# Kernel optimization log

Hardware: AMD Instinct MI355X
Metric: run time of the kernel (lower is better)

## Reference

```python
import jax, jax.numpy as jnp
import numpy as np

D_MODEL = 1024
NUM_HEADS = 16


def setup_inputs() -> dict:
    key = jax.random.key(0)
    ks = jax.random.split(key, 5)
    sigma = (2.0 / (D_MODEL + D_MODEL)) ** 0.5
    def trunc(k):
        # truncated normal in [-3*sigma, 3*sigma], std sigma
        return sigma * jax.random.truncated_normal(k, -3.0, 3.0, (D_MODEL, D_MODEL), jnp.float32)
    x = jax.random.normal(ks[0], (4, 2048, D_MODEL), jnp.float32)
    return {
        "x": x,
        "W_Q": trunc(ks[1]),
        "W_K": trunc(ks[2]),
        "W_V": trunc(ks[3]),
        "W_O": trunc(ks[4]),
    }


def _mha(x, W_Q, W_K, W_V, W_O):
    B, S, D = x.shape
    H = NUM_HEADS
    dk = D // H
    # Linear stores W as (d_out, d_in); einsum '... d_in, d_out d_in -> ... d_out'
    Q = jnp.einsum('bsd,ed->bse', x, W_Q).reshape(B, S, H, dk).transpose(0, 2, 1, 3)
    K = jnp.einsum('bsd,ed->bse', x, W_K).reshape(B, S, H, dk).transpose(0, 2, 1, 3)
    V = jnp.einsum('bsd,ed->bse', x, W_V).reshape(B, S, H, dk).transpose(0, 2, 1, 3)
    scores = jnp.einsum('bhnd,bhmd->bhnm', Q, K) / jnp.sqrt(jnp.asarray(dk, x.dtype))
    causal = jnp.tril(jnp.ones((S, S), bool))
    scores = jnp.where(causal, scores, -jnp.inf)
    attn = jax.nn.softmax(scores, axis=-1)
    out = jnp.einsum('bhnm,bhmd->bhnd', attn, V)  # [B,H,S,dk]
    out = out.transpose(0, 2, 1, 3).reshape(B, S, D)
    return jnp.einsum('bsd,ed->bse', out, W_O)


def reference(x, W_Q, W_K, W_V, W_O):
    return _mha(x, W_Q, W_K, W_V, W_O)
```

## Files before the change

kernel.cpp:

```cpp
#include <hip/hip_runtime.h>
#include <hip/hip_bf16.h>
#include <stdint.h>


typedef unsigned short u16;
typedef short bf16x8 __attribute__((ext_vector_type(8)));
typedef float f32x4 __attribute__((ext_vector_type(4)));
typedef unsigned short u16x8 __attribute__((ext_vector_type(8)));

#define S_LEN 2048
#define DMODEL 1024
#define NH 16

__device__ __forceinline__ u16 f2bf(float f) {
    unsigned u = __builtin_bit_cast(unsigned, f);
    unsigned r = (u + 0x7fffu + ((u >> 16) & 1u)) >> 16;
    return (u16)r;
}

__device__ __forceinline__ float fast_exp2(float x) {
    return __builtin_amdgcn_exp2f(x);
}

__device__ __forceinline__ unsigned cvtpk_bf16(float lo, float hi_) {
    unsigned r;
    asm("v_cvt_pk_bf16_f32 %0, %1, %2" : "=v"(r) : "v"(lo), "v"(hi_));
    return r;
}

__device__ __forceinline__ void gll16(const void* g, void* s) {
    __builtin_amdgcn_global_load_lds((const __attribute__((address_space(1))) unsigned*)g,
                                     (__attribute__((address_space(3))) unsigned*)s, 16, 0, 0);
}

__global__ __launch_bounds__(256) void cast_all(
    const float* __restrict__ x, const float* __restrict__ wq, const float* __restrict__ wk,
    const float* __restrict__ wv, const float* __restrict__ wo,
    u16* __restrict__ xb, u16* __restrict__ wqkv, u16* __restrict__ wob, int nx) {
    const int NW = DMODEL * DMODEL;
    int i4 = (blockIdx.x * 256 + threadIdx.x) * 4;
    const float* src; u16* dst; int off;
    if (i4 < nx)             { src = x;  dst = xb;            off = i4; }
    else if (i4 < nx + NW)   { src = wq; dst = wqkv;          off = i4 - nx; }
    else if (i4 < nx + 2*NW) { src = wk; dst = wqkv + NW;     off = i4 - nx - NW; }
    else if (i4 < nx + 3*NW) { src = wv; dst = wqkv + 2*NW;   off = i4 - nx - 2*NW; }
    else                     { src = wo; dst = wob;           off = i4 - nx - 3*NW; }
    float4 v = *reinterpret_cast<const float4*>(src + off);
    ushort4 o4; o4.x = f2bf(v.x); o4.y = f2bf(v.y); o4.z = f2bf(v.z); o4.w = f2bf(v.w);
    *reinterpret_cast<ushort4*>(dst + off) = o4;
}

template <typename OUT>
__global__ __launch_bounds__(256) void gemm_bt(const u16* __restrict__ A, const u16* __restrict__ B,
                                               OUT* __restrict__ C, int M, int N, int K,
                                               int qcols, float qscale, u16* __restrict__ vt) {
    __shared__ u16 As[128 * 64];
    __shared__ u16 Bs[128 * 64];
    __shared__ u16 Ts[4][16 * 72];
    const int m0 = blockIdx.y * 128, n0 = blockIdx.x * 128;
    const int t = threadIdx.x, w = t >> 6, l = t & 63;
    const int hi = l >> 4;
    const int wr = w >> 1, wc = w & 1;
    f32x4 acc[4][4] = {};

    const int lr = l >> 3;
    const int lc = l & 7;
    const int gcol = (lc ^ lr) * 8;
    const u16* Ag = A + (size_t)(m0 + w * 32 + lr) * K + gcol;
    const u16* Bg = B + (size_t)(n0 + w * 32 + lr) * K + gcol;

    for (int k0 = 0; k0 < K; k0 += 64) {
        __syncthreads();
#pragma unroll
        for (int c = 0; c < 4; c++) {
            gll16(Ag + (size_t)c * 8 * K + k0, As + w * 2048 + c * 512);
            gll16(Bg + (size_t)c * 8 * K + k0, Bs + w * 2048 + c * 512);
        }
        __syncthreads();
#pragma unroll
        for (int kk = 0; kk < 2; kk++) {
            bf16x8 af[4], bfr[4];
#pragma unroll
            for (int mi = 0; mi < 4; mi++)
                af[mi] = *(const bf16x8*)&As[(wr * 64 + mi * 16 + (l & 15)) * 64 +
                                             (((kk * 4 + hi) ^ (l & 7)) * 8)];
#pragma unroll
            for (int ni = 0; ni < 4; ni++)
                bfr[ni] = *(const bf16x8*)&Bs[(wc * 64 + ni * 16 + (l & 15)) * 64 +
                                              (((kk * 4 + hi) ^ (l & 7)) * 8)];
#pragma unroll
            for (int mi = 0; mi < 4; mi++)
#pragma unroll
                for (int ni = 0; ni < 4; ni++)
                    acc[mi][ni] = __builtin_amdgcn_mfma_f32_16x16x32_bf16(af[mi], bfr[ni], acc[mi][ni], 0, 0, 0);
        }
    }

    if (vt != nullptr && n0 >= 2048) {
        const int mw = m0 + wr * 64;
        const int bq = mw >> 11;
        const int s0w = mw & (S_LEN - 1);
        const int hd = ((n0 + wc * 64) - 2048) >> 6;
        u16* tb = &Ts[w][0];
#pragma unroll
        for (int ni = 0; ni < 4; ni++) {
#pragma unroll
            for (int mi = 0; mi < 4; mi++) {
                uint2 pk = make_uint2(cvtpk_bf16(acc[mi][ni][0], acc[mi][ni][1]),
                                      cvtpk_bf16(acc[mi][ni][2], acc[mi][ni][3]));
                *(uint2*)&tb[(l & 15) * 72 + mi * 16 + hi * 4] = pk;
            }
            bf16x8 r0 = *(const bf16x8*)&tb[(l & 15) * 72 + hi * 16];
            bf16x8 r1 = *(const bf16x8*)&tb[(l & 15) * 72 + hi * 16 + 8];
            size_t vrow = ((size_t)(bq * 16 + hd) * 64 + ni * 16 + (l & 15)) * S_LEN + s0w + hi * 16;
            *(u16x8*)&vt[vrow]     = (u16x8)r0;
            *(u16x8*)&vt[vrow + 8] = (u16x8)r1;
        }
    } else {
#pragma unroll
        for (int mi = 0; mi < 4; mi++)
#pragma unroll
            for (int ni = 0; ni < 4; ni++)
#pragma unroll
                for (int j = 0; j < 4; j++) {
                    int r = m0 + wr * 64 + mi * 16 + hi * 4 + j;
                    int c = n0 + wc * 64 + ni * 16 + (l & 15);
                    float v = acc[mi][ni][j];
                    if (c < qcols) v *= qscale;
                    if constexpr (__is_same(OUT, u16)) C[(size_t)r * N + c] = f2bf(v);
                    else                               C[(size_t)r * N + c] = v;
                }
    }
}

__global__ __launch_bounds__(256, 2) void attn(const u16* __restrict__ QKV, const u16* __restrict__ VT,
                                               u16* __restrict__ O) {
    const int bh = blockIdx.x, y = blockIdx.y;
    const int qt = (y < 16) ? y : 47 - y;
    const int b = bh >> 4, h = bh & 15;
    const int t = threadIdx.x, w = t >> 6, l = t & 63;
    const int q = l & 15, hi = l >> 4, s7 = q & 7;

    __shared__ u16 SM[2][2][64][64];
    __shared__ u16 PS[4][16][64];

    const int srow = t >> 3, sblk = t & 7;
    const int gs = (sblk ^ (srow & 7)) * 8;
    const u16* Kg = QKV + (size_t)(b * S_LEN + srow) * 3072 + 1024 + h * 64 + gs;
    const u16* Vg = VT + (size_t)(bh * 64 + srow) * S_LEN + gs;
    const u16* Kg2 = Kg + (size_t)32 * 3072;
    const u16* Vg2 = Vg + (size_t)32 * S_LEN;

    const int kA0 = q * 128 + ((hi ^ s7) << 4);
    const int kA1 = kA0 ^ 64;
    const char* smbase = (const char*)&SM[0][0][0][0];

    char* pbase = (char*)&PS[w][0][0];
    const int pw0 = q * 128 + ((((0 * 2) + (hi >> 1)) ^ s7) << 4) + ((hi & 1) << 3);
    const int pw1 = q * 128 + ((((1 * 2) + (hi >> 1)) ^ s7) << 4) + ((hi & 1) << 3);
    const int pw2 = q * 128 + ((((2 * 2) + (hi >> 1)) ^ s7) << 4) + ((hi & 1) << 3);
    const int pw3 = q * 128 + ((((3 * 2) + (hi >> 1)) ^ s7) << 4) + ((hi & 1) << 3);
    const int pr0 = q * 128 + (((0 * 4 + hi) ^ s7) << 4);
    const int pr1 = q * 128 + (((1 * 4 + hi) ^ s7) << 4);

    const int q64 = qt * 64;
    const int nt = qt + 1;
    const int qglob = q64 + w * 16 + q;

    bf16x8 qf[2];
#pragma unroll
    for (int kk = 0; kk < 2; kk++)
        qf[kk] = *(const bf16x8*)&QKV[(size_t)(b * S_LEN + qglob) * 3072 + h * 64 + kk * 32 + hi * 8];

    f32x4 oacc[4] = {};
    float ss0 = 0.f, ss1 = 0.f;

    gll16(Kg,  (u16*)&SM[0][0][0][0] + t * 8);
    gll16(Kg2, (u16*)&SM[0][0][0][0] + 2048 + t * 8);
    gll16(Vg,  (u16*)&SM[0][1][0][0] + t * 8);
    gll16(Vg2, (u16*)&SM[0][1][0][0] + 2048 + t * 8);
    __syncthreads();

    const u16* KgT  = Kg  + (size_t)64 * 3072;
    const u16* Kg2T = Kg2 + (size_t)64 * 3072;
    const u16* VgT  = Vg  + 64;
    const u16* Vg2T = Vg2 + 64;

#pragma unroll 1
    for (int tt = 0; tt < nt; ++tt) {
        const int cur = tt & 1;
        if (tt + 1 < nt) {
            gll16(KgT,  (u16*)&SM[cur ^ 1][0][0][0] + t * 8);
            gll16(Kg2T, (u16*)&SM[cur ^ 1][0][0][0] + 2048 + t * 8);
            gll16(VgT,  (u16*)&SM[cur ^ 1][1][0][0] + t * 8);
            gll16(Vg2T, (u16*)&SM[cur ^ 1][1][0][0] + 2048 + t * 8);
            KgT  += (size_t)64 * 3072;
            Kg2T += (size_t)64 * 3072;
            VgT  += 64;
            Vg2T += 64;
        }
        const int kv0 = tt * 64;
        const char* kb = smbase + cur * 16384;
        f32x4 sacc[4] = {};
        __builtin_amdgcn_s_setprio(1);
#pragma unroll
        for (int kk = 0; kk < 2; kk++) {
            const char* ka = kb + (kk ? kA1 : kA0);
#pragma unroll
            for (int ni = 0; ni < 4; ni++) {
                bf16x8 kf = *(const bf16x8*)(ka + ni * 2048);
                sacc[ni] = __builtin_amdgcn_mfma_f32_16x16x32_bf16(kf, qf[kk], sacc[ni], 0, 0, 0);
            }
        }
        __builtin_amdgcn_s_setprio(0);
        const int r0 = qglob - kv0;
        if (r0 < 63) {
            const int rth = r0 - hi * 4;
#pragma unroll
            for (int ni = 0; ni < 4; ni++)
#pragma unroll
                for (int j = 0; j < 4; j++)
                    if (ni * 16 + j > rth) sacc[ni][j] = -1e30f;
        }
        float pv[4][4];
#pragma unroll
        for (int ni = 0; ni < 4; ni++)
#pragma unroll
            for (int j = 0; j < 4; j++) pv[ni][j] = fast_exp2(sacc[ni][j] - 8.0f);
        ss0 += ((pv[0][0] + pv[0][1]) + (pv[0][2] + pv[0][3]))
             + ((pv[1][0] + pv[1][1]) + (pv[1][2] + pv[1][3]));
        ss1 += ((pv[2][0] + pv[2][1]) + (pv[2][2] + pv[2][3]))
             + ((pv[3][0] + pv[3][1]) + (pv[3][2] + pv[3][3]));
        *(uint2*)(pbase + pw0) = make_uint2(cvtpk_bf16(pv[0][0], pv[0][1]), cvtpk_bf16(pv[0][2], pv[0][3]));
        *(uint2*)(pbase + pw1) = make_uint2(cvtpk_bf16(pv[1][0], pv[1][1]), cvtpk_bf16(pv[1][2], pv[1][3]));
        *(uint2*)(pbase + pw2) = make_uint2(cvtpk_bf16(pv[2][0], pv[2][1]), cvtpk_bf16(pv[2][2], pv[2][3]));
        *(uint2*)(pbase + pw3) = make_uint2(cvtpk_bf16(pv[3][0], pv[3][1]), cvtpk_bf16(pv[3][2], pv[3][3]));
        bf16x8 pf0 = *(const bf16x8*)(pbase + pr0);
        bf16x8 pf1 = *(const bf16x8*)(pbase + pr1);
        const char* vb = kb + 8192;
        __builtin_amdgcn_s_setprio(1);
#pragma unroll
        for (int kk = 0; kk < 2; kk++) {
            const char* va = vb + (kk ? kA1 : kA0);
            bf16x8 pf = kk ? pf1 : pf0;
#pragma unroll
            for (int di = 0; di < 4; di++) {
                bf16x8 vf = *(const bf16x8*)(va + di * 2048);
                oacc[di] = __builtin_amdgcn_mfma_f32_16x16x32_bf16(vf, pf, oacc[di], 0, 0, 0);
            }
        }
        __builtin_amdgcn_s_setprio(0);
        __syncthreads();
    }

    float ssr = ss0 + ss1;
    ssr += __shfl_xor(ssr, 16, 64);
    ssr += __shfl_xor(ssr, 32, 64);
    float inv = 1.0f / ssr;
#pragma unroll
    for (int di = 0; di < 4; di++) {
        ushort4 o4;
        o4.x = f2bf(oacc[di][0] * inv);
        o4.y = f2bf(oacc[di][1] * inv);
        o4.z = f2bf(oacc[di][2] * inv);
        o4.w = f2bf(oacc[di][3] * inv);
        *(ushort4*)&O[(size_t)(b * S_LEN + qglob) * DMODEL + h * 64 + di * 16 + hi * 4] = o4;
    }
}

extern "C" void kernel_launch(void* const* d_in, const int* in_sizes, int n_in,
                              void* d_out, int out_size, void* d_ws, size_t ws_size,
                              hipStream_t stream) {
    const float* x  = (const float*)d_in[0];
    const float* wq = (const float*)d_in[1];
    const float* wk = (const float*)d_in[2];
    const float* wv = (const float*)d_in[3];
    const float* wo = (const float*)d_in[4];
    const int nx = in_sizes[0];
    const int BS = nx / DMODEL;
    const int NW = DMODEL * DMODEL;

    u16* xb   = (u16*)d_ws;
    u16* wqkv = xb + (size_t)nx;
    u16* wob  = wqkv + (size_t)3 * NW;
    u16* qkv  = wob + (size_t)NW;
    u16* vt   = qkv + (size_t)BS * 3072;
    u16* ob   = vt + (size_t)nx;

    int ncast = (nx + 4 * NW) / 4 / 256;
    cast_all<<<ncast, 256, 0, stream>>>(x, wq, wk, wv, wo, xb, wqkv, wob, nx);

    const float QSC = 0.125f * 1.44269504088896f;
    gemm_bt<u16><<<dim3(3072 / 128, BS / 128), 256, 0, stream>>>(xb, wqkv, qkv, BS, 3072, DMODEL,
                                                                 DMODEL, QSC, vt);

    attn<<<dim3((BS / S_LEN) * NH, 32), 256, 0, stream>>>(qkv, vt, ob);

    gemm_bt<float><<<dim3(DMODEL / 128, BS / 128), 256, 0, stream>>>(ob, wob, (float*)d_out, BS, DMODEL, DMODEL,
                                                                     0, 1.0f, nullptr);
}
```

Baseline: 160.8 us.

## Process two 64-row query tiles per attention block to reuse K/V tiles

Each attention workgroup now handles a 128-row query slab as two 64-row sub-tiles (A and B) that share every K/V tile staged in shared memory. This halves the grid and the number of K/V global loads and barriers per query row. Sub-tile A's MFMAs and softmax are skipped on the final key tile, where it is fully masked. The launch-bounds hint rises to 4 blocks per CU, while per-thread register use roughly doubles, which may cause spills or limit occupancy.

```diff
diff --git a/kernel.cpp b/kernel.cpp
--- a/kernel.cpp
+++ b/kernel.cpp
@@ -133,10 +133,10 @@
     }
 }
 
-__global__ __launch_bounds__(256, 2) void attn(const u16* __restrict__ QKV, const u16* __restrict__ VT,
+__global__ __launch_bounds__(256, 4) void attn(const u16* __restrict__ QKV, const u16* __restrict__ VT,
                                                u16* __restrict__ O) {
     const int bh = blockIdx.x, y = blockIdx.y;
-    const int qt = (y < 16) ? y : 47 - y;
+    const int p = (y < 8) ? y : 23 - y;
     const int b = bh >> 4, h = bh & 15;
     const int t = threadIdx.x, w = t >> 6, l = t & 63;
     const int q = l & 15, hi = l >> 4, s7 = q & 7;
@@ -163,17 +163,20 @@
     const int pr0 = q * 128 + (((0 * 4 + hi) ^ s7) << 4);
     const int pr1 = q * 128 + (((1 * 4 + hi) ^ s7) << 4);
 
-    const int q64 = qt * 64;
-    const int nt = qt + 1;
-    const int qglob = q64 + w * 16 + q;
-
-    bf16x8 qf[2];
-#pragma unroll
-    for (int kk = 0; kk < 2; kk++)
-        qf[kk] = *(const bf16x8*)&QKV[(size_t)(b * S_LEN + qglob) * 3072 + h * 64 + kk * 32 + hi * 8];
-
-    f32x4 oacc[4] = {};
-    float ss0 = 0.f, ss1 = 0.f;
+    const int q128 = p * 128;
+    const int nt = 2 * p + 2;
+    const int qgA = q128 + w * 16 + q;
+    const int qgB = qgA + 64;
+
+    bf16x8 qfA[2], qfB[2];
+#pragma unroll
+    for (int kk = 0; kk < 2; kk++) {
+        qfA[kk] = *(const bf16x8*)&QKV[(size_t)(b * S_LEN + qgA) * 3072 + h * 64 + kk * 32 + hi * 8];
+        qfB[kk] = *(const bf16x8*)&QKV[(size_t)(b * S_LEN + qgB) * 3072 + h * 64 + kk * 32 + hi * 8];
+    }
+
+    f32x4 oaccA[4] = {}, oaccB[4] = {};
+    float ssA0 = 0.f, ssA1 = 0.f, ssB0 = 0.f, ssB1 = 0.f;
 
     gll16(Kg,  (u16*)&SM[0][0][0][0] + t * 8);
     gll16(Kg2, (u16*)&SM[0][0][0][0] + 2048 + t * 8);
@@ -200,8 +203,10 @@
             Vg2T += 64;
         }
         const int kv0 = tt * 64;
+        const bool actA = (q128 + w * 16 + 15 >= kv0);
         const char* kb = smbase + cur * 16384;
-        f32x4 sacc[4] = {};
+
+        f32x4 saccA[4] = {}, saccB[4] = {};
         __builtin_amdgcn_s_setprio(1);
 #pragma unroll
         for (int kk = 0; kk < 2; kk++) {
@@ -209,62 +214,116 @@
 #pragma unroll
             for (int ni = 0; ni < 4; ni++) {
                 bf16x8 kf = *(const bf16x8*)(ka + ni * 2048);
-                sacc[ni] = __builtin_amdgcn_mfma_f32_16x16x32_bf16(kf, qf[kk], sacc[ni], 0, 0, 0);
+                if (actA)
+                    saccA[ni] = __builtin_amdgcn_mfma_f32_16x16x32_bf16(kf, qfA[kk], saccA[ni], 0, 0, 0);
+                saccB[ni] = __builtin_amdgcn_mfma_f32_16x16x32_bf16(kf, qfB[kk], saccB[ni], 0, 0, 0);
             }
         }
         __builtin_amdgcn_s_setprio(0);
-        const int r0 = qglob - kv0;
-        if (r0 < 63) {
-            const int rth = r0 - hi * 4;
+
+        bf16x8 pfA0, pfA1, pfB0, pfB1;
+        if (actA) {
+            const int r0 = qgA - kv0;
+            if (r0 < 63) {
+                const int rth = r0 - hi * 4;
+#pragma unroll
+                for (int ni = 0; ni < 4; ni++)
+#pragma unroll
+                    for (int j = 0; j < 4; j++)
+                        if (ni * 16 + j > rth) saccA[ni][j] = -1e30f;
+            }
+            float pv[4][4];
 #pragma unroll
             for (int ni = 0; ni < 4; ni++)
 #pragma unroll
-                for (int j = 0; j < 4; j++)
-                    if (ni * 16 + j > rth) sacc[ni][j] = -1e30f;
-        }
-        float pv[4][4];
-#pragma unroll
-        for (int ni = 0; ni < 4; ni++)
-#pragma unroll
-            for (int j = 0; j < 4; j++) pv[ni][j] = fast_exp2(sacc[ni][j] - 8.0f);
-        ss0 += ((pv[0][0] + pv[0][1]) + (pv[0][2] + pv[0][3]))
-             + ((pv[1][0] + pv[1][1]) + (pv[1][2] + pv[1][3]));
-        ss1 += ((pv[2][0] + pv[2][1]) + (pv[2][2] + pv[2][3]))
-             + ((pv[3][0] + pv[3][1]) + (pv[3][2] + pv[3][3]));
-        *(uint2*)(pbase + pw0) = make_uint2(cvtpk_bf16(pv[0][0], pv[0][1]), cvtpk_bf16(pv[0][2], pv[0][3]));
-        *(uint2*)(pbase + pw1) = make_uint2(cvtpk_bf16(pv[1][0], pv[1][1]), cvtpk_bf16(pv[1][2], pv[1][3]));
-        *(uint2*)(pbase + pw2) = make_uint2(cvtpk_bf16(pv[2][0], pv[2][1]), cvtpk_bf16(pv[2][2], pv[2][3]));
-        *(uint2*)(pbase + pw3) = make_uint2(cvtpk_bf16(pv[3][0], pv[3][1]), cvtpk_bf16(pv[3][2], pv[3][3]));
-        bf16x8 pf0 = *(const bf16x8*)(pbase + pr0);
-        bf16x8 pf1 = *(const bf16x8*)(pbase + pr1);
+                for (int j = 0; j < 4; j++) pv[ni][j] = fast_exp2(saccA[ni][j] - 8.0f);
+            ssA0 += ((pv[0][0] + pv[0][1]) + (pv[0][2] + pv[0][3]))
+                  + ((pv[1][0] + pv[1][1]) + (pv[1][2] + pv[1][3]));
+            ssA1 += ((pv[2][0] + pv[2][1]) + (pv[2][2] + pv[2][3]))
+                  + ((pv[3][0] + pv[3][1]) + (pv[3][2] + pv[3][3]));
+            *(uint2*)(pbase + pw0) = make_uint2(cvtpk_bf16(pv[0][0], pv[0][1]), cvtpk_bf16(pv[0][2], pv[0][3]));
+            *(uint2*)(pbase + pw1) = make_uint2(cvtpk_bf16(pv[1][0], pv[1][1]), cvtpk_bf16(pv[1][2], pv[1][3]));
+            *(uint2*)(pbase + pw2) = make_uint2(cvtpk_bf16(pv[2][0], pv[2][1]), cvtpk_bf16(pv[2][2], pv[2][3]));
+            *(uint2*)(pbase + pw3) = make_uint2(cvtpk_bf16(pv[3][0], pv[3][1]), cvtpk_bf16(pv[3][2], pv[3][3]));
+            pfA0 = *(const bf16x8*)(pbase + pr0);
+            pfA1 = *(const bf16x8*)(pbase + pr1);
+        }
+        {
+            const int r0 = qgB - kv0;
+            if (r0 < 63) {
+                const int rth = r0 - hi * 4;
+#pragma unroll
+                for (int ni = 0; ni < 4; ni++)
+#pragma unroll
+                    for (int j = 0; j < 4; j++)
+                        if (ni * 16 + j > rth) saccB[ni][j] = -1e30f;
+            }
+            float pv[4][4];
+#pragma unroll
+            for (int ni = 0; ni < 4; ni++)
+#pragma unroll
+                for (int j = 0; j < 4; j++) pv[ni][j] = fast_exp2(saccB[ni][j] - 8.0f);
+            ssB0 += ((pv[0][0] + pv[0][1]) + (pv[0][2] + pv[0][3]))
+                  + ((pv[1][0] + pv[1][1]) + (pv[1][2] + pv[1][3]));
+            ssB1 += ((pv[2][0] + pv[2][1]) + (pv[2][2] + pv[2][3]))
+                  + ((pv[3][0] + pv[3][1]) + (pv[3][2] + pv[3][3]));
+            *(uint2*)(pbase + pw0) = make_uint2(cvtpk_bf16(pv[0][0], pv[0][1]), cvtpk_bf16(pv[0][2], pv[0][3]));
+            *(uint2*)(pbase + pw1) = make_uint2(cvtpk_bf16(pv[1][0], pv[1][1]), cvtpk_bf16(pv[1][2], pv[1][3]));
+            *(uint2*)(pbase + pw2) = make_uint2(cvtpk_bf16(pv[2][0], pv[2][1]), cvtpk_bf16(pv[2][2], pv[2][3]));
+            *(uint2*)(pbase + pw3) = make_uint2(cvtpk_bf16(pv[3][0], pv[3][1]), cvtpk_bf16(pv[3][2], pv[3][3]));
+            pfB0 = *(const bf16x8*)(pbase + pr0);
+            pfB1 = *(const bf16x8*)(pbase + pr1);
+        }
+
         const char* vb = kb + 8192;
         __builtin_amdgcn_s_setprio(1);
 #pragma unroll
         for (int kk = 0; kk < 2; kk++) {
             const char* va = vb + (kk ? kA1 : kA0);
-            bf16x8 pf = kk ? pf1 : pf0;
 #pragma unroll
             for (int di = 0; di < 4; di++) {
                 bf16x8 vf = *(const bf16x8*)(va + di * 2048);
-                oacc[di] = __builtin_amdgcn_mfma_f32_16x16x32_bf16(vf, pf, oacc[di], 0, 0, 0);
+                if (actA) {
+                    bf16x8 pfa = kk ? pfA1 : pfA0;
+                    oaccA[di] = __builtin_amdgcn_mfma_f32_16x16x32_bf16(vf, pfa, oaccA[di], 0, 0, 0);
+                }
+                bf16x8 pfb = kk ? pfB1 : pfB0;
+                oaccB[di] = __builtin_amdgcn_mfma_f32_16x16x32_bf16(vf, pfb, oaccB[di], 0, 0, 0);
             }
         }
         __builtin_amdgcn_s_setprio(0);
         __syncthreads();
     }
 
-    float ssr = ss0 + ss1;
-    ssr += __shfl_xor(ssr, 16, 64);
-    ssr += __shfl_xor(ssr, 32, 64);
-    float inv = 1.0f / ssr;
-#pragma unroll
-    for (int di = 0; di < 4; di++) {
-        ushort4 o4;
-        o4.x = f2bf(oacc[di][0] * inv);
-        o4.y = f2bf(oacc[di][1] * inv);
-        o4.z = f2bf(oacc[di][2] * inv);
-        o4.w = f2bf(oacc[di][3] * inv);
-        *(ushort4*)&O[(size_t)(b * S_LEN + qglob) * DMODEL + h * 64 + di * 16 + hi * 4] = o4;
+    {
+        float ssr = ssA0 + ssA1;
+        ssr += __shfl_xor(ssr, 16, 64);
+        ssr += __shfl_xor(ssr, 32, 64);
+        float inv = 1.0f / ssr;
+#pragma unroll
+        for (int di = 0; di < 4; di++) {
+            ushort4 o4;
+            o4.x = f2bf(oaccA[di][0] * inv);
+            o4.y = f2bf(oaccA[di][1] * inv);
+            o4.z = f2bf(oaccA[di][2] * inv);
+            o4.w = f2bf(oaccA[di][3] * inv);
+            *(ushort4*)&O[(size_t)(b * S_LEN + qgA) * DMODEL + h * 64 + di * 16 + hi * 4] = o4;
+        }
+    }
+    {
+        float ssr = ssB0 + ssB1;
+        ssr += __shfl_xor(ssr, 16, 64);
+        ssr += __shfl_xor(ssr, 32, 64);
+        float inv = 1.0f / ssr;
+#pragma unroll
+        for (int di = 0; di < 4; di++) {
+            ushort4 o4;
+            o4.x = f2bf(oaccB[di][0] * inv);
+            o4.y = f2bf(oaccB[di][1] * inv);
+            o4.z = f2bf(oaccB[di][2] * inv);
+            o4.w = f2bf(oaccB[di][3] * inv);
+            *(ushort4*)&O[(size_t)(b * S_LEN + qgB) * DMODEL + h * 64 + di * 16 + hi * 4] = o4;
+        }
     }
 }
 
@@ -294,7 +353,7 @@
     gemm_bt<u16><<<dim3(3072 / 128, BS / 128), 256, 0, stream>>>(xb, wqkv, qkv, BS, 3072, DMODEL,
                                                                  DMODEL, QSC, vt);
 
-    attn<<<dim3((BS / S_LEN) * NH, 32), 256, 0, stream>>>(qkv, vt, ob);
+    attn<<<dim3((BS / S_LEN) * NH, 16), 256, 0, stream>>>(qkv, vt, ob);
 
     gemm_bt<float><<<dim3(DMODEL / 128, BS / 128), 256, 0, stream>>>(ob, wob, (float*)d_out, BS, DMODEL, DMODEL,
                                                                      0, 1.0f, nullptr);
```

Result: slower. 509.3 us (+216.8%).
